# Performance work log

Measured on AMD Instinct MI355X. Metric: run time of the kernel, lower is better.

Reference implementation:

```python
import jax, jax.numpy as jnp
from jax import lax
import numpy as np

SEQ_LEN, INPUT_DIM, NUM_HIDDEN, NUM_CLASSES, BATCH = 512, 64, 128, 10, 1024


def setup_inputs() -> dict:
    key = jax.random.key(0)
    ks = jax.random.split(key, 12)
    bound = float(np.sqrt(1.0 / NUM_HIDDEN))

    def u(k, shape):
        return jax.random.uniform(k, shape, jnp.float32, -bound, bound)

    return {
        "x": jax.random.normal(ks[0], (BATCH, SEQ_LEN, INPUT_DIM), jnp.float32),
        "W_gx": u(ks[1], (INPUT_DIM, NUM_HIDDEN)),
        "W_gh": u(ks[2], (NUM_HIDDEN, NUM_HIDDEN)),
        "W_ix": u(ks[3], (INPUT_DIM, NUM_HIDDEN)),
        "W_ih": u(ks[4], (NUM_HIDDEN, NUM_HIDDEN)),
        "W_fx": u(ks[5], (INPUT_DIM, NUM_HIDDEN)),
        "W_fh": u(ks[6], (NUM_HIDDEN, NUM_HIDDEN)),
        "W_ox": u(ks[7], (INPUT_DIM, NUM_HIDDEN)),
        "W_oh": u(ks[8], (NUM_HIDDEN, NUM_HIDDEN)),
        "W_ph": u(ks[9], (NUM_HIDDEN, NUM_CLASSES)),
        "b_g": jnp.zeros((NUM_HIDDEN,), jnp.float32),
        "b_i": jnp.zeros((NUM_HIDDEN,), jnp.float32),
        "b_f": jnp.ones((NUM_HIDDEN,), jnp.float32),  # forget-gate bias init to 1 as in original
        "b_o": jnp.zeros((NUM_HIDDEN,), jnp.float32),
        "b_p": jnp.zeros((NUM_CLASSES,), jnp.float32),
    }


def reference(x, W_gx, W_gh, W_ix, W_ih, W_fx, W_fh, W_ox, W_oh, W_ph,
              b_g, b_i, b_f, b_o, b_p):
    B, T, D = x.shape
    H = W_gh.shape[0]

    def step(carry, x_t):  # x_t: [B, D]
        h, c = carry
        g = jnp.tanh(x_t @ W_gx + h @ W_gh + b_g)
        i = jax.nn.sigmoid(x_t @ W_ix + h @ W_ih + b_i)
        f = jax.nn.sigmoid(x_t @ W_fx + h @ W_fh + b_f)
        o = jax.nn.sigmoid(x_t @ W_ox + h @ W_oh + b_o)
        c = g * i + c * f
        h = jnp.tanh(c) * o
        return (h, c), None

    h0 = jnp.zeros((B, H), x.dtype)
    c0 = jnp.zeros((B, H), x.dtype)
    (h, c), _ = lax.scan(step, (h0, c0), jnp.swapaxes(x, 0, 1))  # scan over time
    return h @ W_ph + b_p  # [B, num_classes]
```

## Files before the change

kernel.cpp:

```cpp
#include <hip/hip_runtime.h>

#define BATCH 1024
#define TSEQ  512
#define DIN   64
#define H     128
#define NCLS  10
#define BM    16
#define NTHREADS 512

typedef _Float16 h16;
typedef __attribute__((ext_vector_type(4))) _Float16 half4v;
typedef __attribute__((ext_vector_type(8))) _Float16 half8v;
typedef __attribute__((ext_vector_type(4))) float f32x4;

__device__ __forceinline__ int stg_addr(int m, int k) {
    const int kg = k >> 3;
    return (((kg << 4) + (m ^ (kg & 7))) << 3) + (k & 7);
}

__device__ __forceinline__ half4v pack4(float a, float b, float c, float d) {
    half4v v;
    v[0] = (h16)a; v[1] = (h16)b; v[2] = (h16)c; v[3] = (h16)d;
    return v;
}

__device__ __forceinline__ float sigm_pre(float y) {
    return __builtin_amdgcn_rcpf(1.f + __builtin_amdgcn_exp2f(y));
}

#define SCALE_G (-2.8853900817779268f)
#define SCALE_S (-1.4426950408889634f)

__global__ __launch_bounds__(NTHREADS, 2)
void lstm_persist(const float* __restrict__ x,
                  const float* __restrict__ Wgx, const float* __restrict__ Wgh,
                  const float* __restrict__ Wix, const float* __restrict__ Wih,
                  const float* __restrict__ Wfx, const float* __restrict__ Wfh,
                  const float* __restrict__ Wox, const float* __restrict__ Woh,
                  const float* __restrict__ Wph,
                  const float* __restrict__ bg, const float* __restrict__ bi,
                  const float* __restrict__ bfg, const float* __restrict__ bo,
                  const float* __restrict__ bp,
                  float* __restrict__ out)
{
    __shared__ __align__(16) h16 hbuf[2][H * BM];
    __shared__ __align__(16) h16 xbuf[2][DIN * BM];

    const int tid  = threadIdx.x;
    const int wave = tid >> 6;
    const int lane = tid & 63;
    const int grp  = lane >> 4;
    const int ln   = lane & 15;
    const int b0   = blockIdx.x * BM;
    const int n    = (wave << 4) + ln;

    half8v bx[4][2];
    half8v bh[4][4];
    f32x4  bias_c[4];
    {
        const float* WX[4] = {Wgx, Wix, Wfx, Wox};
        const float* WH[4] = {Wgh, Wih, Wfh, Woh};
        const float* BB[4] = {bg, bi, bfg, bo};
        const float  SC[4] = {SCALE_G, SCALE_S, SCALE_S, SCALE_S};
        #pragma unroll
        for (int G = 0; G < 4; ++G) {
            #pragma unroll
            for (int s = 0; s < 2; ++s) {
                half8v v;
                #pragma unroll
                for (int j = 0; j < 8; ++j)
                    v[j] = (h16)(WX[G][(32*s + 8*grp + j) * H + n] * SC[G]);
                bx[G][s] = v;
            }
            #pragma unroll
            for (int s = 0; s < 4; ++s) {
                half8v v;
                #pragma unroll
                for (int j = 0; j < 8; ++j)
                    v[j] = (h16)(WH[G][(32*s + 8*grp + j) * H + n] * SC[G]);
                bh[G][s] = v;
            }
            const float bb = BB[G][n] * SC[G];
            bias_c[G] = (f32x4){bb, bb, bb, bb};
        }
    }

    const int ha0 = stg_addr(ln,      8 * grp);
    const int ha1 = stg_addr(ln, 32 + 8 * grp);
    const int ha2 = stg_addr(ln, 64 + 8 * grp);
    const int ha3 = stg_addr(ln, 96 + 8 * grp);
    const int xa0 = ha0;
    const int xa1 = ha1;
    int hwr[4];
    #pragma unroll
    for (int r = 0; r < 4; ++r) hwr[r] = stg_addr((grp << 2) + r, n);

    const int xm  = tid >> 4;
    const int xk0 = (tid & 15) << 2;
    const int xwr = stg_addr(xm, xk0);
    const float* xrow = x + (size_t)(b0 + xm) * TSEQ * DIN + xk0;

    *(half4v*)&hbuf[0][tid << 2] = (half4v)0;
    if (tid < 256) {
        f32x4 x0 = *(const f32x4*)xrow;
        *(half4v*)&xbuf[0][xwr] = pack4(x0[0], x0[1], x0[2], x0[3]);
    }
    __syncthreads();

    f32x4 accA[4], accB[4];
    {
        half8v xf0 = *(const half8v*)&xbuf[0][xa0];
        half8v xf1 = *(const half8v*)&xbuf[0][xa1];
        #pragma unroll
        for (int G = 0; G < 4; ++G) {
            accA[G] = __builtin_amdgcn_mfma_f32_16x16x32_f16(xf0, bx[G][0], bias_c[G], 0, 0, 0);
            accA[G] = __builtin_amdgcn_mfma_f32_16x16x32_f16(xf1, bx[G][1], accA[G], 0, 0, 0);
        }
    }
    __syncthreads();

    f32x4 xhold = {0.f, 0.f, 0.f, 0.f};
    f32x4 xnew  = {0.f, 0.f, 0.f, 0.f};
    if (tid < 256) {
        f32x4 x1 = *(const f32x4*)(xrow + DIN);
        *(half4v*)&xbuf[0][xwr] = pack4(x1[0], x1[1], x1[2], x1[3]);
        xhold = *(const f32x4*)(xrow + 2 * DIN);
        xnew  = *(const f32x4*)(xrow + 3 * DIN);
    }

    f32x4 cstate = {0.f, 0.f, 0.f, 0.f};

#define STEP(p_, tcur, ACCC, ACCN)                                              \
  {                                                                             \
    __syncthreads();                                                            \
    half8v ah0 = *(const half8v*)&hbuf[p_][ha0];                                \
    half8v ah1 = *(const half8v*)&hbuf[p_][ha1];                                \
    half8v ah2 = *(const half8v*)&hbuf[p_][ha2];                                \
    half8v ah3 = *(const half8v*)&hbuf[p_][ha3];                                \
    half8v xf0 = *(const half8v*)&xbuf[p_][xa0];                 \
    half8v xf1 = *(const half8v*)&xbuf[p_][xa1];                                \
    _Pragma("unroll")                                                           \
    for (int G = 0; G < 4; ++G) {                                               \
        ACCC[G] = __builtin_amdgcn_mfma_f32_16x16x32_f16(ah0, bh[G][0], ACCC[G], 0, 0, 0); \
        ACCC[G] = __builtin_amdgcn_mfma_f32_16x16x32_f16(ah1, bh[G][1], ACCC[G], 0, 0, 0); \
        ACCC[G] = __builtin_amdgcn_mfma_f32_16x16x32_f16(ah2, bh[G][2], ACCC[G], 0, 0, 0); \
        ACCC[G] = __builtin_amdgcn_mfma_f32_16x16x32_f16(ah3, bh[G][3], ACCC[G], 0, 0, 0); \
    }                                                                           \
    _Pragma("unroll")                                                           \
    for (int G = 0; G < 4; ++G) {                                               \
        ACCN[G] = __builtin_amdgcn_mfma_f32_16x16x32_f16(xf0, bx[G][0], bias_c[G], 0, 0, 0); \
        ACCN[G] = __builtin_amdgcn_mfma_f32_16x16x32_f16(xf1, bx[G][1], ACCN[G], 0, 0, 0); \
    }                                                                           \
               \
    if (tid < 256) {                                                            \
        *(half4v*)&xbuf[p_ ^ 1][xwr] = pack4(xhold[0], xhold[1], xhold[2], xhold[3]); \
        xhold = xnew;                                                           \
        const int tpre = ((tcur) + 4 < TSEQ) ? (tcur) + 4 : TSEQ - 1;           \
        xnew = *(const f32x4*)(xrow + (size_t)tpre * DIN);                      \
    }                                                                           \
                    \
    f32x4 hv;                                                                   \
    _Pragma("unroll")                                                           \
    for (int r = 0; r < 4; ++r) {                                               \
        float gv = __builtin_fmaf(2.f, sigm_pre(ACCC[0][r]), -1.f);             \
        float iv = sigm_pre(ACCC[1][r]);                                        \
        float fv = sigm_pre(ACCC[2][r]);                                        \
        float ov = sigm_pre(ACCC[3][r]);                                        \
        float c  = __builtin_fmaf(cstate[r], fv, gv * iv);                      \
        cstate[r] = c;                                                          \
        float tc = __builtin_fmaf(2.f, sigm_pre(c * SCALE_G), -1.f);            \
        hv[r] = tc * ov;                                                        \
    }                                                                           \
    h16* hw = hbuf[p_ ^ 1];                                                     \
    _Pragma("unroll")                                                           \
    for (int r = 0; r < 4; ++r)                                                 \
        hw[hwr[r]] = (h16)hv[r];                                                \
  }

    for (int t = 0; t < TSEQ; t += 2) {
        STEP(0, t,     accA, accB)
        STEP(1, t + 1, accB, accA)
    }
#undef STEP

    __syncthreads();
    if (tid < BM * NCLS) {
        const int m = tid / NCLS;
        const int cls = tid - m * NCLS;
        float s = bp[cls];
        #pragma unroll 8
        for (int k = 0; k < H; ++k) {
            float hvv = (float)hbuf[0][stg_addr(m, k)];
            s += hvv * Wph[k * NCLS + cls];
        }
        out[(size_t)(b0 + m) * NCLS + cls] = s;
    }
}

extern "C" void kernel_launch(void* const* d_in, const int* in_sizes, int n_in,
                              void* d_out, int out_size, void* d_ws, size_t ws_size,
                              hipStream_t stream) {
    (void)in_sizes; (void)n_in; (void)d_ws; (void)ws_size; (void)out_size;
    lstm_persist<<<dim3(BATCH / BM), dim3(NTHREADS), 0, stream>>>(
        (const float*)d_in[0],
        (const float*)d_in[1], (const float*)d_in[2],
        (const float*)d_in[3], (const float*)d_in[4],
        (const float*)d_in[5], (const float*)d_in[6],
        (const float*)d_in[7], (const float*)d_in[8],
        (const float*)d_in[9],
        (const float*)d_in[10], (const float*)d_in[11],
        (const float*)d_in[12], (const float*)d_in[13],
        (const float*)d_in[14],
        (float*)d_out);
}
```

Measured before the change: 429.4 us.

## Interleave per-gate MFMA chains with activation math and spread x staging over all threads

Each LSTM step now issues the recurrent MFMA chain one gate at a time and computes that gate's activation while the next gate's MFMAs run, so transcendental ALU work overlaps matrix-core latency on the serial critical path. The x prefetch is moved to the start of the step and uses all 512 threads, each loading two floats, which removes the tid<256 branch. The input-projection MFMAs for the next step are moved after the cell update. This relies on the compiler keeping the written order, and it changes register pressure.

```diff
diff --git a/kernel.cpp b/kernel.cpp
--- a/kernel.cpp
+++ b/kernel.cpp
@@ -9,8 +9,10 @@
 #define NTHREADS 512
 
 typedef _Float16 h16;
+typedef __attribute__((ext_vector_type(2))) _Float16 half2v;
 typedef __attribute__((ext_vector_type(4))) _Float16 half4v;
 typedef __attribute__((ext_vector_type(8))) _Float16 half8v;
+typedef __attribute__((ext_vector_type(2))) float f32x2;
 typedef __attribute__((ext_vector_type(4))) float f32x4;
 
 __device__ __forceinline__ int stg_addr(int m, int k) {
@@ -18,18 +20,14 @@
     return (((kg << 4) + (m ^ (kg & 7))) << 3) + (k & 7);
 }
 
-__device__ __forceinline__ half4v pack4(float a, float b, float c, float d) {
-    half4v v;
-    v[0] = (h16)a; v[1] = (h16)b; v[2] = (h16)c; v[3] = (h16)d;
-    return v;
-}
-
 __device__ __forceinline__ float sigm_pre(float y) {
     return __builtin_amdgcn_rcpf(1.f + __builtin_amdgcn_exp2f(y));
 }
 
 #define SCALE_G (-2.8853900817779268f)
 #define SCALE_S (-1.4426950408889634f)
+
+#define MFMA16(A, B, C) __builtin_amdgcn_mfma_f32_16x16x32_f16((A), (B), (C), 0, 0, 0)
 
 __global__ __launch_bounds__(NTHREADS, 2)
 void lstm_persist(const float* __restrict__ x,
@@ -95,15 +93,16 @@
     #pragma unroll
     for (int r = 0; r < 4; ++r) hwr[r] = stg_addr((grp << 2) + r, n);
 
-    const int xm  = tid >> 4;
-    const int xk0 = (tid & 15) << 2;
+    const int xm  = tid >> 5;
+    const int xk0 = (tid & 31) << 1;
     const int xwr = stg_addr(xm, xk0);
     const float* xrow = x + (size_t)(b0 + xm) * TSEQ * DIN + xk0;
 
     *(half4v*)&hbuf[0][tid << 2] = (half4v)0;
-    if (tid < 256) {
-        f32x4 x0 = *(const f32x4*)xrow;
-        *(half4v*)&xbuf[0][xwr] = pack4(x0[0], x0[1], x0[2], x0[3]);
+    {
+        f32x2 x0 = *(const f32x2*)xrow;
+        half2v w; w[0] = (h16)x0[0]; w[1] = (h16)x0[1];
+        *(half2v*)&xbuf[0][xwr] = w;
     }
     __syncthreads();
 
@@ -113,19 +112,19 @@
         half8v xf1 = *(const half8v*)&xbuf[0][xa1];
         #pragma unroll
         for (int G = 0; G < 4; ++G) {
-            accA[G] = __builtin_amdgcn_mfma_f32_16x16x32_f16(xf0, bx[G][0], bias_c[G], 0, 0, 0);
-            accA[G] = __builtin_amdgcn_mfma_f32_16x16x32_f16(xf1, bx[G][1], accA[G], 0, 0, 0);
+            accA[G] = MFMA16(xf0, bx[G][0], bias_c[G]);
+            accA[G] = MFMA16(xf1, bx[G][1], accA[G]);
         }
     }
     __syncthreads();
 
-    f32x4 xhold = {0.f, 0.f, 0.f, 0.f};
-    f32x4 xnew  = {0.f, 0.f, 0.f, 0.f};
-    if (tid < 256) {
-        f32x4 x1 = *(const f32x4*)(xrow + DIN);
-        *(half4v*)&xbuf[0][xwr] = pack4(x1[0], x1[1], x1[2], x1[3]);
-        xhold = *(const f32x4*)(xrow + 2 * DIN);
-        xnew  = *(const f32x4*)(xrow + 3 * DIN);
+    f32x2 xhold, xnew;
+    {
+        f32x2 x1 = *(const f32x2*)(xrow + DIN);
+        half2v w; w[0] = (h16)x1[0]; w[1] = (h16)x1[1];
+        *(half2v*)&xbuf[0][xwr] = w;
+        xhold = *(const f32x2*)(xrow + 2 * DIN);
+        xnew  = *(const f32x2*)(xrow + 3 * DIN);
     }
 
     f32x4 cstate = {0.f, 0.f, 0.f, 0.f};
@@ -133,48 +132,69 @@
 #define STEP(p_, tcur, ACCC, ACCN)                                              \
   {                                                                             \
     __syncthreads();                                                            \
+                \
+    const int tpre = ((tcur) + 4 < TSEQ) ? (tcur) + 4 : TSEQ - 1;               \
+    f32x2 xpre = *(const f32x2*)(xrow + (size_t)tpre * DIN);                    \
+                                                                 \
     half8v ah0 = *(const half8v*)&hbuf[p_][ha0];                                \
     half8v ah1 = *(const half8v*)&hbuf[p_][ha1];                                \
     half8v ah2 = *(const half8v*)&hbuf[p_][ha2];                                \
     half8v ah3 = *(const half8v*)&hbuf[p_][ha3];                                \
     half8v xf0 = *(const half8v*)&xbuf[p_][xa0];                 \
     half8v xf1 = *(const half8v*)&xbuf[p_][xa1];                                \
+                    \
+    { half2v w; w[0] = (h16)xhold[0]; w[1] = (h16)xhold[1];                     \
+      *(half2v*)&xbuf[p_ ^ 1][xwr] = w; }                                       \
+    xhold = xnew; xnew = xpre;                                                  \
+                                                              \
+    ACCC[0] = MFMA16(ah0, bh[0][0], ACCC[0]);                                   \
+    ACCC[0] = MFMA16(ah1, bh[0][1], ACCC[0]);                                   \
+    ACCC[0] = MFMA16(ah2, bh[0][2], ACCC[0]);                                   \
+    ACCC[0] = MFMA16(ah3, bh[0][3], ACCC[0]);                                   \
+                                                              \
+    ACCC[1] = MFMA16(ah0, bh[1][0], ACCC[1]);                                   \
+    ACCC[1] = MFMA16(ah1, bh[1][1], ACCC[1]);                                   \
+    ACCC[1] = MFMA16(ah2, bh[1][2], ACCC[1]);                                   \
+    ACCC[1] = MFMA16(ah3, bh[1][3], ACCC[1]);                                   \
+                                       \
+    f32x4 gv, iv, fv, ov, pv, tc;                                               \
+    _Pragma("unroll")                                                           \
+    for (int r = 0; r < 4; ++r)                                                 \
+        gv[r] = __builtin_fmaf(2.f, sigm_pre(ACCC[0][r]), -1.f);                \
+                                                              \
+    ACCC[2] = MFMA16(ah0, bh[2][0], ACCC[2]);                                   \
+    ACCC[2] = MFMA16(ah1, bh[2][1], ACCC[2]);                                   \
+    ACCC[2] = MFMA16(ah2, bh[2][2], ACCC[2]);                                   \
+    ACCC[2] = MFMA16(ah3, bh[2][3], ACCC[2]);                                   \
+    _Pragma("unroll")                                                           \
+    for (int r = 0; r < 4; ++r) {                                               \
+        iv[r] = sigm_pre(ACCC[1][r]);                                           \
+        pv[r] = gv[r] * iv[r];                                                  \
+    }                                                                           \
+                                                              \
+    ACCC[3] = MFMA16(ah0, bh[3][0], ACCC[3]);                                   \
+    ACCC[3] = MFMA16(ah1, bh[3][1], ACCC[3]);                                   \
+    ACCC[3] = MFMA16(ah2, bh[3][2], ACCC[3]);                                   \
+    ACCC[3] = MFMA16(ah3, bh[3][3], ACCC[3]);                                   \
+    _Pragma("unroll")                                                           \
+    for (int r = 0; r < 4; ++r) {                                               \
+        fv[r] = sigm_pre(ACCC[2][r]);                                           \
+        float c = __builtin_fmaf(cstate[r], fv[r], pv[r]);                      \
+        cstate[r] = c;                                                          \
+        tc[r] = __builtin_fmaf(2.f, sigm_pre(c * SCALE_G), -1.f);               \
+    }                                                                           \
+          \
     _Pragma("unroll")                                                           \
     for (int G = 0; G < 4; ++G) {                                               \
-        ACCC[G] = __builtin_amdgcn_mfma_f32_16x16x32_f16(ah0, bh[G][0], ACCC[G], 0, 0, 0); \
-        ACCC[G] = __builtin_amdgcn_mfma_f32_16x16x32_f16(ah1, bh[G][1], ACCC[G], 0, 0, 0); \
-        ACCC[G] = __builtin_amdgcn_mfma_f32_16x16x32_f16(ah2, bh[G][2], ACCC[G], 0, 0, 0); \
-        ACCC[G] = __builtin_amdgcn_mfma_f32_16x16x32_f16(ah3, bh[G][3], ACCC[G], 0, 0, 0); \
-    }                                                                           \
-    _Pragma("unroll")                                                           \
-    for (int G = 0; G < 4; ++G) {                                               \
-        ACCN[G] = __builtin_amdgcn_mfma_f32_16x16x32_f16(xf0, bx[G][0], bias_c[G], 0, 0, 0); \
-        ACCN[G] = __builtin_amdgcn_mfma_f32_16x16x32_f16(xf1, bx[G][1], ACCN[G], 0, 0, 0); \
-    }                                                                           \
-               \
-    if (tid < 256) {                                                            \
-        *(half4v*)&xbuf[p_ ^ 1][xwr] = pack4(xhold[0], xhold[1], xhold[2], xhold[3]); \
-        xhold = xnew;                                                           \
-        const int tpre = ((tcur) + 4 < TSEQ) ? (tcur) + 4 : TSEQ - 1;           \
-        xnew = *(const f32x4*)(xrow + (size_t)tpre * DIN);                      \
-    }                                                                           \
-                    \
-    f32x4 hv;                                                                   \
+        ACCN[G] = MFMA16(xf0, bx[G][0], bias_c[G]);                             \
+        ACCN[G] = MFMA16(xf1, bx[G][1], ACCN[G]);                               \
+    }                                                                           \
+    h16* hw = hbuf[p_ ^ 1];                                                     \
     _Pragma("unroll")                                                           \
     for (int r = 0; r < 4; ++r) {                                               \
-        float gv = __builtin_fmaf(2.f, sigm_pre(ACCC[0][r]), -1.f);             \
-        float iv = sigm_pre(ACCC[1][r]);                                        \
-        float fv = sigm_pre(ACCC[2][r]);                                        \
-        float ov = sigm_pre(ACCC[3][r]);                                        \
-        float c  = __builtin_fmaf(cstate[r], fv, gv * iv);                      \
-        cstate[r] = c;                                                          \
-        float tc = __builtin_fmaf(2.f, sigm_pre(c * SCALE_G), -1.f);            \
-        hv[r] = tc * ov;                                                        \
-    }                                                                           \
-    h16* hw = hbuf[p_ ^ 1];                                                     \
-    _Pragma("unroll")                                                           \
-    for (int r = 0; r < 4; ++r)                                                 \
-        hw[hwr[r]] = (h16)hv[r];                                                \
+        ov[r] = sigm_pre(ACCC[3][r]);                                           \
+        hw[hwr[r]] = (h16)(tc[r] * ov[r]);                                      \
+    }                                                                           \
   }
 
     for (int t = 0; t < TSEQ; t += 2) {
```

After: 404.9 us. 1.06x faster.

## Halve block to 4 waves each computing two N-tiles, fuse gate reciprocals

Applied to the files above, without the earlier changes.

Cuts the block from 8 waves to 4, so each wave now owns two 16-column N-tiles and keeps twice the weight fragments in registers. The input-projection MFMAs and the x staging move ahead of the barrier so they overlap the wait. The gate math merges several sigmoid/tanh reciprocals into one shared rcp per cell update and one per hidden output, and clamps the tanh exponent to avoid overflow. The aim is cheaper barriers, fewer transcendental ops and more independent MFMAs per wave. The cost is higher register pressure, lower occupancy (launch bounds 1) and slightly different rounding.

```diff
diff --git a/kernel.cpp b/kernel.cpp
--- a/kernel.cpp
+++ b/kernel.cpp
@@ -6,11 +6,13 @@
 #define H     128
 #define NCLS  10
 #define BM    16
-#define NTHREADS 512
+#define NTHREADS 256
 
 typedef _Float16 h16;
+typedef __attribute__((ext_vector_type(2))) _Float16 half2v;
 typedef __attribute__((ext_vector_type(4))) _Float16 half4v;
 typedef __attribute__((ext_vector_type(8))) _Float16 half8v;
+typedef __attribute__((ext_vector_type(2))) float f32x2;
 typedef __attribute__((ext_vector_type(4))) float f32x4;
 
 __device__ __forceinline__ int stg_addr(int m, int k) {
@@ -18,20 +20,12 @@
     return (((kg << 4) + (m ^ (kg & 7))) << 3) + (k & 7);
 }
 
-__device__ __forceinline__ half4v pack4(float a, float b, float c, float d) {
-    half4v v;
-    v[0] = (h16)a; v[1] = (h16)b; v[2] = (h16)c; v[3] = (h16)d;
-    return v;
-}
-
-__device__ __forceinline__ float sigm_pre(float y) {
-    return __builtin_amdgcn_rcpf(1.f + __builtin_amdgcn_exp2f(y));
-}
-
 #define SCALE_G (-2.8853900817779268f)
 #define SCALE_S (-1.4426950408889634f)
 
-__global__ __launch_bounds__(NTHREADS, 2)
+#define MFMA16(A, B, C) __builtin_amdgcn_mfma_f32_16x16x32_f16((A), (B), (C), 0, 0, 0)
+
+__global__ __launch_bounds__(NTHREADS, 1)
 void lstm_persist(const float* __restrict__ x,
                   const float* __restrict__ Wgx, const float* __restrict__ Wgh,
                   const float* __restrict__ Wix, const float* __restrict__ Wih,
@@ -52,36 +46,41 @@
     const int grp  = lane >> 4;
     const int ln   = lane & 15;
     const int b0   = blockIdx.x * BM;
-    const int n    = (wave << 4) + ln;
-
-    half8v bx[4][2];
-    half8v bh[4][4];
-    f32x4  bias_c[4];
+    const int n0   = (wave << 5) + ln;
+    const int n1   = n0 + 16;
+
+    half8v bx[4][2][2];
+    half8v bh[4][4][2];
+    f32x4  bias_c[4][2];
     {
         const float* WX[4] = {Wgx, Wix, Wfx, Wox};
         const float* WH[4] = {Wgh, Wih, Wfh, Woh};
         const float* BB[4] = {bg, bi, bfg, bo};
         const float  SC[4] = {SCALE_G, SCALE_S, SCALE_S, SCALE_S};
+        const int    nn[2] = {n0, n1};
         #pragma unroll
         for (int G = 0; G < 4; ++G) {
             #pragma unroll
-            for (int s = 0; s < 2; ++s) {
-                half8v v;
+            for (int nt = 0; nt < 2; ++nt) {
                 #pragma unroll
-                for (int j = 0; j < 8; ++j)
-                    v[j] = (h16)(WX[G][(32*s + 8*grp + j) * H + n] * SC[G]);
-                bx[G][s] = v;
+                for (int s = 0; s < 2; ++s) {
+                    half8v v;
+                    #pragma unroll
+                    for (int j = 0; j < 8; ++j)
+                        v[j] = (h16)(WX[G][(32*s + 8*grp + j) * H + nn[nt]] * SC[G]);
+                    bx[G][s][nt] = v;
+                }
+                #pragma unroll
+                for (int s = 0; s < 4; ++s) {
+                    half8v v;
+                    #pragma unroll
+                    for (int j = 0; j < 8; ++j)
+                        v[j] = (h16)(WH[G][(32*s + 8*grp + j) * H + nn[nt]] * SC[G]);
+                    bh[G][s][nt] = v;
+                }
+                const float bb = BB[G][nn[nt]] * SC[G];
+                bias_c[G][nt] = (f32x4){bb, bb, bb, bb};
             }
-            #pragma unroll
-            for (int s = 0; s < 4; ++s) {
-                half8v v;
-                #pragma unroll
-                for (int j = 0; j < 8; ++j)
-                    v[j] = (h16)(WH[G][(32*s + 8*grp + j) * H + n] * SC[G]);
-                bh[G][s] = v;
-            }
-            const float bb = BB[G][n] * SC[G];
-            bias_c[G] = (f32x4){bb, bb, bb, bb};
         }
     }
 
@@ -91,90 +90,140 @@
     const int ha3 = stg_addr(ln, 96 + 8 * grp);
     const int xa0 = ha0;
     const int xa1 = ha1;
-    int hwr[4];
+    int hwr[2][4];
     #pragma unroll
-    for (int r = 0; r < 4; ++r) hwr[r] = stg_addr((grp << 2) + r, n);
+    for (int r = 0; r < 4; ++r) {
+        hwr[0][r] = stg_addr((grp << 2) + r, n0);
+        hwr[1][r] = stg_addr((grp << 2) + r, n1);
+    }
 
     const int xm  = tid >> 4;
     const int xk0 = (tid & 15) << 2;
     const int xwr = stg_addr(xm, xk0);
     const float* xrow = x + (size_t)(b0 + xm) * TSEQ * DIN + xk0;
 
-    *(half4v*)&hbuf[0][tid << 2] = (half4v)0;
-    if (tid < 256) {
+    *(half8v*)&hbuf[0][tid << 3] = (half8v)0;
+    {
         f32x4 x0 = *(const f32x4*)xrow;
-        *(half4v*)&xbuf[0][xwr] = pack4(x0[0], x0[1], x0[2], x0[3]);
-    }
-    __syncthreads();
-
-    f32x4 accA[4], accB[4];
+        half4v w; w[0] = (h16)x0[0]; w[1] = (h16)x0[1]; w[2] = (h16)x0[2]; w[3] = (h16)x0[3];
+        *(half4v*)&xbuf[0][xwr] = w;
+    }
+    __syncthreads();
+
+    f32x4 accA[4][2], accB[4][2];
     {
         half8v xf0 = *(const half8v*)&xbuf[0][xa0];
         half8v xf1 = *(const half8v*)&xbuf[0][xa1];
         #pragma unroll
-        for (int G = 0; G < 4; ++G) {
-            accA[G] = __builtin_amdgcn_mfma_f32_16x16x32_f16(xf0, bx[G][0], bias_c[G], 0, 0, 0);
-            accA[G] = __builtin_amdgcn_mfma_f32_16x16x32_f16(xf1, bx[G][1], accA[G], 0, 0, 0);
-        }
-    }
-    __syncthreads();
-
-    f32x4 xhold = {0.f, 0.f, 0.f, 0.f};
-    f32x4 xnew  = {0.f, 0.f, 0.f, 0.f};
-    if (tid < 256) {
+        for (int G = 0; G < 4; ++G)
+            #pragma unroll
+            for (int nt = 0; nt < 2; ++nt) {
+                accA[G][nt] = MFMA16(xf0, bx[G][0][nt], bias_c[G][nt]);
+                accA[G][nt] = MFMA16(xf1, bx[G][1][nt], accA[G][nt]);
+            }
+    }
+    __syncthreads();
+
+    f32x4 xhold, xnew;
+    {
         f32x4 x1 = *(const f32x4*)(xrow + DIN);
-        *(half4v*)&xbuf[0][xwr] = pack4(x1[0], x1[1], x1[2], x1[3]);
+        half4v w; w[0] = (h16)x1[0]; w[1] = (h16)x1[1]; w[2] = (h16)x1[2]; w[3] = (h16)x1[3];
+        *(half4v*)&xbuf[0][xwr] = w;
         xhold = *(const f32x4*)(xrow + 2 * DIN);
         xnew  = *(const f32x4*)(xrow + 3 * DIN);
     }
-
-    f32x4 cstate = {0.f, 0.f, 0.f, 0.f};
+    __syncthreads();
+
+    f32x4 cstate[2] = {{0.f,0.f,0.f,0.f},{0.f,0.f,0.f,0.f}};
 
 #define STEP(p_, tcur, ACCC, ACCN)                                              \
   {                                                                             \
+                    \
+    half8v xf0 = *(const half8v*)&xbuf[p_][xa0];                 \
+    half8v xf1 = *(const half8v*)&xbuf[p_][xa1];                                \
+    { half4v w; w[0] = (h16)xhold[0]; w[1] = (h16)xhold[1];                     \
+      w[2] = (h16)xhold[2]; w[3] = (h16)xhold[3];                               \
+      *(half4v*)&xbuf[p_ ^ 1][xwr] = w; }                  \
+    xhold = xnew;                                                               \
+    const int tpre = ((tcur) + 4 < TSEQ) ? (tcur) + 4 : TSEQ - 1;               \
+    xnew = *(const f32x4*)(xrow + (size_t)tpre * DIN);                          \
+    _Pragma("unroll")                                                           \
+    for (int G = 0; G < 4; ++G)                                                 \
+        _Pragma("unroll")                                                       \
+        for (int nt = 0; nt < 2; ++nt) {                                        \
+            ACCN[G][nt] = MFMA16(xf0, bx[G][0][nt], bias_c[G][nt]);             \
+            ACCN[G][nt] = MFMA16(xf1, bx[G][1][nt], ACCN[G][nt]);               \
+        }                                                                       \
     __syncthreads();                                                            \
+                                                       \
     half8v ah0 = *(const half8v*)&hbuf[p_][ha0];                                \
     half8v ah1 = *(const half8v*)&hbuf[p_][ha1];                                \
     half8v ah2 = *(const half8v*)&hbuf[p_][ha2];                                \
     half8v ah3 = *(const half8v*)&hbuf[p_][ha3];                                \
-    half8v xf0 = *(const half8v*)&xbuf[p_][xa0];                 \
-    half8v xf1 = *(const half8v*)&xbuf[p_][xa1];                                \
+             \
+    ACCC[0][0] = MFMA16(ah0, bh[0][0][0], ACCC[0][0]);                          \
+    ACCC[0][1] = MFMA16(ah0, bh[0][0][1], ACCC[0][1]);                          \
+    ACCC[1][0] = MFMA16(ah0, bh[1][0][0], ACCC[1][0]);                          \
+    ACCC[1][1] = MFMA16(ah0, bh[1][0][1], ACCC[1][1]);                          \
+    ACCC[2][0] = MFMA16(ah0, bh[2][0][0], ACCC[2][0]);                          \
+    ACCC[2][1] = MFMA16(ah0, bh[2][0][1], ACCC[2][1]);                          \
+    ACCC[0][0] = MFMA16(ah1, bh[0][1][0], ACCC[0][0]);                          \
+    ACCC[0][1] = MFMA16(ah1, bh[0][1][1], ACCC[0][1]);                          \
+    ACCC[1][0] = MFMA16(ah1, bh[1][1][0], ACCC[1][0]);                          \
+    ACCC[1][1] = MFMA16(ah1, bh[1][1][1], ACCC[1][1]);                          \
+    ACCC[2][0] = MFMA16(ah1, bh[2][1][0], ACCC[2][0]);                          \
+    ACCC[2][1] = MFMA16(ah1, bh[2][1][1], ACCC[2][1]);                          \
+    ACCC[0][0] = MFMA16(ah2, bh[0][2][0], ACCC[0][0]);                          \
+    ACCC[0][1] = MFMA16(ah2, bh[0][2][1], ACCC[0][1]);                          \
+    ACCC[1][0] = MFMA16(ah2, bh[1][2][0], ACCC[1][0]);                          \
+    ACCC[1][1] = MFMA16(ah2, bh[1][2][1], ACCC[1][1]);                          \
+    ACCC[2][0] = MFMA16(ah2, bh[2][2][0], ACCC[2][0]);                          \
+    ACCC[2][1] = MFMA16(ah2, bh[2][2][1], ACCC[2][1]);                          \
+    ACCC[0][0] = MFMA16(ah3, bh[0][3][0], ACCC[0][0]);                          \
+    ACCC[0][1] = MFMA16(ah3, bh[0][3][1], ACCC[0][1]);                          \
+    ACCC[1][0] = MFMA16(ah3, bh[1][3][0], ACCC[1][0]);                          \
+    ACCC[1][1] = MFMA16(ah3, bh[1][3][1], ACCC[1][1]);                          \
+    ACCC[2][0] = MFMA16(ah3, bh[2][3][0], ACCC[2][0]);                          \
+    ACCC[2][1] = MFMA16(ah3, bh[2][3][1], ACCC[2][1]);                          \
+                                    \
+    ACCC[3][0] = MFMA16(ah0, bh[3][0][0], ACCC[3][0]);                          \
+    ACCC[3][1] = MFMA16(ah0, bh[3][0][1], ACCC[3][1]);                          \
+    ACCC[3][0] = MFMA16(ah1, bh[3][1][0], ACCC[3][0]);                          \
+    ACCC[3][1] = MFMA16(ah1, bh[3][1][1], ACCC[3][1]);                          \
+    ACCC[3][0] = MFMA16(ah2, bh[3][2][0], ACCC[3][0]);                          \
+    ACCC[3][1] = MFMA16(ah2, bh[3][2][1], ACCC[3][1]);                          \
+    ACCC[3][0] = MFMA16(ah3, bh[3][3][0], ACCC[3][0]);                          \
+    ACCC[3][1] = MFMA16(ah3, bh[3][3][1], ACCC[3][1]);                          \
+               \
+    f32x4 ycv[2];                                                               \
     _Pragma("unroll")                                                           \
-    for (int G = 0; G < 4; ++G) {                                               \
-        ACCC[G] = __builtin_amdgcn_mfma_f32_16x16x32_f16(ah0, bh[G][0], ACCC[G], 0, 0, 0); \
-        ACCC[G] = __builtin_amdgcn_mfma_f32_16x16x32_f16(ah1, bh[G][1], ACCC[G], 0, 0, 0); \
-        ACCC[G] = __builtin_amdgcn_mfma_f32_16x16x32_f16(ah2, bh[G][2], ACCC[G], 0, 0, 0); \
-        ACCC[G] = __builtin_amdgcn_mfma_f32_16x16x32_f16(ah3, bh[G][3], ACCC[G], 0, 0, 0); \
-    }                                                                           \
-    _Pragma("unroll")                                                           \
-    for (int G = 0; G < 4; ++G) {                                               \
-        ACCN[G] = __builtin_amdgcn_mfma_f32_16x16x32_f16(xf0, bx[G][0], bias_c[G], 0, 0, 0); \
-        ACCN[G] = __builtin_amdgcn_mfma_f32_16x16x32_f16(xf1, bx[G][1], ACCN[G], 0, 0, 0); \
-    }                                                                           \
-               \
-    if (tid < 256) {                                                            \
-        *(half4v*)&xbuf[p_ ^ 1][xwr] = pack4(xhold[0], xhold[1], xhold[2], xhold[3]); \
-        xhold = xnew;                                                           \
-        const int tpre = ((tcur) + 4 < TSEQ) ? (tcur) + 4 : TSEQ - 1;           \
-        xnew = *(const f32x4*)(xrow + (size_t)tpre * DIN);                      \
-    }                                                                           \
+    for (int nt = 0; nt < 2; ++nt)                                              \
+        _Pragma("unroll")                                                       \
+        for (int r = 0; r < 4; ++r) {                                           \
+            float eg = __builtin_amdgcn_exp2f(ACCC[0][nt][r]);                  \
+            float ei = __builtin_amdgcn_exp2f(ACCC[1][nt][r]);                  \
+            float ef = __builtin_amdgcn_exp2f(ACCC[2][nt][r]);                  \
+            float ag = 1.f + eg;                                                \
+            float ai = 1.f + ei;                                                \
+            float af = 1.f + ef;                                                \
+            float dp  = ag * ai;                                                \
+            float num = __builtin_fmaf(cstate[nt][r], dp, (1.f - eg) * af);     \
+            float c   = num * __builtin_amdgcn_rcpf(dp * af);                   \
+            cstate[nt][r] = c;                                                  \
+            ycv[nt][r] = fminf(c * SCALE_G, 126.f);                             \
+        }                                                                       \
                     \
-    f32x4 hv;                                                                   \
-    _Pragma("unroll")                                                           \
-    for (int r = 0; r < 4; ++r) {                                               \
-        float gv = __builtin_fmaf(2.f, sigm_pre(ACCC[0][r]), -1.f);             \
-        float iv = sigm_pre(ACCC[1][r]);                                        \
-        float fv = sigm_pre(ACCC[2][r]);                                        \
-        float ov = sigm_pre(ACCC[3][r]);                                        \
-        float c  = __builtin_fmaf(cstate[r], fv, gv * iv);                      \
-        cstate[r] = c;                                                          \
-        float tc = __builtin_fmaf(2.f, sigm_pre(c * SCALE_G), -1.f);            \
-        hv[r] = tc * ov;                                                        \
-    }                                                                           \
     h16* hw = hbuf[p_ ^ 1];                                                     \
     _Pragma("unroll")                                                           \
-    for (int r = 0; r < 4; ++r)                                                 \
-        hw[hwr[r]] = (h16)hv[r];                                                \
+    for (int nt = 0; nt < 2; ++nt)                                              \
+        _Pragma("unroll")                                                       \
+        for (int r = 0; r < 4; ++r) {                                           \
+            float ec = __builtin_amdgcn_exp2f(ycv[nt][r]);                      \
+            float eo = __builtin_amdgcn_exp2f(ACCC[3][nt][r]);                  \
+            float dh = (1.f + ec) * (1.f + eo);                                 \
+            float hv = (1.f - ec) * __builtin_amdgcn_rcpf(dh);                  \
+            hw[hwr[nt][r]] = (h16)hv;                                           \
+        }                                                                       \
   }
 
     for (int t = 0; t < TSEQ; t += 2) {
```

Measured after the change: 515.8 us. 20.1% more time.
